# Kernel tuning notes

Measured on AMD Instinct MI355X. Metric: run time of the kernel, lower is better.

Reference implementation:

```python
import jax, jax.numpy as jnp
import numpy as np

BATCH, SEQ, DIM, NH = 2, 4096, 1024, 16
HD = DIM // NH
BLOCK = 64


def setup_inputs() -> dict:
    key = jax.random.key(0)
    ks = jax.random.split(key, 8)
    x = jax.random.normal(ks[0], (BATCH, SEQ, DIM), dtype=jnp.float32)
    # standard RoPE tables: (seq, head_dim)
    inv_freq = 1.0 / (10000.0 ** (jnp.arange(0, HD, 2, dtype=jnp.float32) / HD))
    t = jnp.arange(SEQ, dtype=jnp.float32)
    freqs = jnp.outer(t, inv_freq)                      # (SEQ, HD//2)
    emb = jnp.concatenate([freqs, freqs], axis=-1)      # (SEQ, HD)
    cos, sin = jnp.cos(emb), jnp.sin(emb)
    s = 0.02
    wq = jax.random.normal(ks[1], (DIM, DIM), jnp.float32) * s
    wk = jax.random.normal(ks[2], (DIM, DIM), jnp.float32) * s
    wv = jax.random.normal(ks[3], (DIM, DIM), jnp.float32) * s
    wo = jax.random.normal(ks[4], (DIM, DIM), jnp.float32) * s
    A_log = jax.random.normal(ks[5], (NH,), jnp.float32) * 0.1
    w_dt_w = jax.random.normal(ks[6], (DIM, NH), jnp.float32) * s
    w_dt_b = jnp.zeros((NH,), jnp.float32)
    return {"x": x, "cos": cos, "sin": sin, "wq": wq, "wk": wk, "wv": wv,
            "wo": wo, "A_log": A_log, "w_dt_w": w_dt_w, "w_dt_b": w_dt_b}


def segsum(a):
    """a: (..., T) -> (..., T, T) lower-triangular segment sums, -inf above diag."""
    T = a.shape[-1]
    cs = jnp.cumsum(a, axis=-1)
    seg = cs[..., :, None] - cs[..., None, :]
    mask = jnp.tril(jnp.ones((T, T), dtype=bool))
    return jnp.where(mask, seg, -jnp.inf)


def rotate_half(t):
    t1, t2 = jnp.split(t, 2, axis=-1)
    return jnp.concatenate([-t2, t1], axis=-1)


def ssd(X, A, B, C, block_len):
    """Mamba-2 SSD chunked scan.
    X: (b,l,h,p)  A: (b,l,h)  B,C: (b,l,h,n)
    """
    b, l, h, p = X.shape
    c = l // block_len
    Xc = X.reshape(b, c, block_len, h, p)
    Bc = B.reshape(b, c, block_len, h, -1)
    Cc = C.reshape(b, c, block_len, h, -1)
    Ac = jnp.transpose(A.reshape(b, c, block_len, h), (0, 3, 1, 2))  # (b,h,c,l)
    A_cumsum = jnp.cumsum(Ac, axis=-1)
    # intra-chunk (diagonal block) output
    L = jnp.exp(segsum(Ac))                                          # (b,h,c,l,l)
    Y_diag = jnp.einsum('bclhn,bcshn,bhcls,bcshp->bclhp', Cc, Bc, L, Xc)
    # per-chunk states
    decay_states = jnp.exp(A_cumsum[:, :, :, -1:] - A_cumsum)        # (b,h,c,l)
    states = jnp.einsum('bclhn,bhcl,bclhp->bchpn', Bc, decay_states, Xc)
    init = jnp.zeros_like(states[:, :1])
    states = jnp.concatenate([init, states], axis=1)                 # (b,c+1,h,p,n)
    # inter-chunk recurrence (done as a 1-SS matmul over chunk axis)
    A_last = jnp.pad(A_cumsum[:, :, :, -1], ((0, 0), (0, 0), (1, 0)))
    decay_chunk = jnp.exp(segsum(A_last))                            # (b,h,c+1,c+1)
    new_states = jnp.einsum('bhzc,bchpn->bzhpn', decay_chunk, states)
    states, final_state = new_states[:, :-1], new_states[:, -1]
    # state -> output contribution
    state_decay_out = jnp.exp(A_cumsum)
    Y_off = jnp.einsum('bclhn,bchpn,bhcl->bclhp', Cc, states, state_decay_out)
    Y = (Y_diag + Y_off).reshape(b, l, h, p)
    return Y, final_state


def reference(x, cos, sin, wq, wk, wv, wo, A_log, w_dt_w, w_dt_b):
    b, l, dim = x.shape
    h = A_log.shape[0]
    d = dim // h
    xq = (x @ wq).reshape(b, l, h, d)
    xk = (x @ wk).reshape(b, l, h, d)
    xv = (x @ wv).reshape(b, l, h, d)
    cb = cos[None, :, None, :]
    sb = sin[None, :, None, :]
    xq = xq * cb + rotate_half(xq) * sb
    xk = xk * cb + rotate_half(xk) * sb
    dt = jax.nn.softplus(x @ w_dt_w + w_dt_b)           # (b,l,h)
    A = -jnp.exp(A_log)[None, None, :] * dt             # (b,l,h)
    X = xv * dt[..., None]                              # (b,l,h,d)
    Y, state = ssd(X, A, xk, xq, BLOCK)
    # replicate torch's transpose(1,2).view(b, l, -1) exactly:
    y = jnp.transpose(Y, (0, 2, 1, 3)).reshape(b, l, h * d)
    return y @ wo, state
```

## Files before the change

### kernel.cpp

```cpp
#include <hip/hip_runtime.h>


typedef __bf16 bf16x8 __attribute__((ext_vector_type(8)));
typedef float f32x4 __attribute__((ext_vector_type(4)));
typedef unsigned int u32x4 __attribute__((ext_vector_type(4)));
typedef unsigned short u16x8 __attribute__((ext_vector_type(8)));
typedef unsigned short u16x4 __attribute__((ext_vector_type(4)));

__device__ __forceinline__ unsigned short f2bf(float f) {
  unsigned int u = __builtin_bit_cast(unsigned int, f);
  u += 0x7fffu + ((u >> 16) & 1u);
  return (unsigned short)(u >> 16);
}
__device__ __forceinline__ float bf2f(unsigned short s) {
  unsigned int u = ((unsigned int)s) << 16;
  return __builtin_bit_cast(float, u);
}

#define GLOAD16(gp, lp)                                                \
  __builtin_amdgcn_global_load_lds(                                    \
      (const __attribute__((address_space(1))) void*)(gp),             \
      (__attribute__((address_space(3))) void*)(lp), 16, 0, 0)

__global__ __launch_bounds__(256) void convert_bf16_kernel(
    const float* __restrict__ in, unsigned short* __restrict__ out, int n4) {
  int g = blockIdx.x * 256 + threadIdx.x;
  if (g < n4) {
    f32x4 v = *reinterpret_cast<const f32x4*>(in + (size_t)g * 4);
    u16x4 o;
    o.x = f2bf(v.x); o.y = f2bf(v.y); o.z = f2bf(v.z); o.w = f2bf(v.w);
    *reinterpret_cast<u16x4*>(out + (size_t)g * 4) = o;
  }
}

__global__ __launch_bounds__(256) void transpose_w_kernel(
    const float* __restrict__ w0, const float* __restrict__ w1,
    const float* __restrict__ w2, const float* __restrict__ w3,
    unsigned short* __restrict__ wt) {
  __shared__ float tile[32][33];
  const int z = blockIdx.z;
  const float* w = (z == 0) ? w0 : (z == 1) ? w1 : (z == 2) ? w2 : w3;
  unsigned short* o = wt + (size_t)z * 1024 * 1024;
  const int bx = blockIdx.x, by = blockIdx.y;
  const int tx = threadIdx.x, ty = threadIdx.y;
#pragma unroll
  for (int i = 0; i < 4; ++i)
    tile[ty + i * 8][tx] = w[(size_t)(by * 32 + ty + i * 8) * 1024 + bx * 32 + tx];
  __syncthreads();
#pragma unroll
  for (int i = 0; i < 4; ++i)
    o[(size_t)(bx * 32 + ty + i * 8) * 1024 + by * 32 + tx] = f2bf(tile[tx][ty + i * 8]);
}

__global__ __launch_bounds__(256) void wdt_t_kernel(
    const float* __restrict__ wdt, unsigned short* __restrict__ out) {
  const int g = blockIdx.x * 256 + threadIdx.x;
  const int n = g >> 10, k = g & 1023;
  out[g] = f2bf(wdt[k * 16 + n]);
}

__global__ __launch_bounds__(256) void dt_gemm_kernel(
    const unsigned short* __restrict__ A,
    const unsigned short* __restrict__ Bt,
    const float* __restrict__ bdt, float* __restrict__ dt) {
  __shared__ unsigned short As[2 * 64 * 32];
  const int tid = threadIdx.x, lane = tid & 63, w = tid >> 6;
  const int m0 = blockIdx.x * 64;
  const unsigned short* ga =
      A + (size_t)(m0 + w * 16 + (lane >> 2)) * 1024 + (lane & 3) * 8;
  unsigned short* la = As + w * 512;
  const int lr = lane & 15, lk = (lane >> 4) * 8;
  const unsigned short* gb = Bt + (size_t)lr * 1024 + lk;
  f32x4 acc = {};
  for (int kt = 0; kt < 1024; kt += 64) {
    GLOAD16(ga + kt, la);
    GLOAD16(ga + kt + 32, la + 2048);
    bf16x8 bF0 = *reinterpret_cast<const bf16x8*>(gb + kt);
    bf16x8 bF1 = *reinterpret_cast<const bf16x8*>(gb + kt + 32);
    __syncthreads();
    bf16x8 aF0 = *reinterpret_cast<const bf16x8*>(&As[(w * 16 + lr) * 32 + lk]);
    bf16x8 aF1 = *reinterpret_cast<const bf16x8*>(&As[2048 + (w * 16 + lr) * 32 + lk]);
    acc = __builtin_amdgcn_mfma_f32_16x16x32_bf16(aF0, bF0, acc, 0, 0, 0);
    acc = __builtin_amdgcn_mfma_f32_16x16x32_bf16(aF1, bF1, acc, 0, 0, 0);
    __syncthreads();
  }
  const int h = lr;
  const float bv = bdt[h];
#pragma unroll
  for (int r = 0; r < 4; ++r) {
    const int row = m0 + w * 16 + (lane >> 4) * 4 + r;
    const float a = acc[r] + bv;
    const float sp = (a > 0.f) ? (a + log1pf(expf(-a))) : log1pf(expf(a));
    dt[(size_t)row * 16 + h] = sp;
  }
}

template <int EPI>
__global__ __launch_bounds__(256) void gemm128_kernel(
    const unsigned short* __restrict__ A, const unsigned short* __restrict__ Bt,
    void* __restrict__ outp, const float* __restrict__ cosb,
    const float* __restrict__ sinb, const float* __restrict__ dtb) {
  __shared__ unsigned short As[128 * 32];
  __shared__ unsigned short Bs[128 * 32];
  const int tid = threadIdx.x, lane = tid & 63, w = tid >> 6;
  const int m0 = blockIdx.y * 128, n0 = blockIdx.x * 128;
  const int srow = w * 32 + (lane >> 2);
  const int scol = (lane & 3) * 8;
  const unsigned short* ga = A + (size_t)(m0 + srow) * 1024 + scol;
  const unsigned short* gb = Bt + (size_t)(n0 + srow) * 1024 + scol;
  unsigned short* la = As + (w * 32) * 32;
  unsigned short* lb = Bs + (w * 32) * 32;
  const int lr = lane & 15, lk = (lane >> 4) * 8;
  const int wr = w >> 1, wc = w & 1;
  f32x4 acc[4][4] = {};
  for (int kt = 0; kt < 1024; kt += 32) {
    GLOAD16(ga + kt, la);
    GLOAD16(ga + kt + (size_t)16 * 1024, la + 16 * 32);
    GLOAD16(gb + kt, lb);
    GLOAD16(gb + kt + (size_t)16 * 1024, lb + 16 * 32);
    __syncthreads();
    bf16x8 aF[4], bF[4];
#pragma unroll
    for (int i = 0; i < 4; ++i) {
      aF[i] = *reinterpret_cast<const bf16x8*>(&As[(wr * 64 + i * 16 + lr) * 32 + lk]);
      bF[i] = *reinterpret_cast<const bf16x8*>(&Bs[(wc * 64 + i * 16 + lr) * 32 + lk]);
    }
#pragma unroll
    for (int i = 0; i < 4; ++i)
#pragma unroll
      for (int j = 0; j < 4; ++j)
        acc[i][j] = __builtin_amdgcn_mfma_f32_16x16x32_bf16(aF[i], bF[j], acc[i][j], 0, 0, 0);
    __syncthreads();
  }
  const int r0 = m0 + wr * 64 + ((lane >> 4) << 2);
  const int c0 = n0 + wc * 64 + lr;
  if constexpr (EPI == 0) {
    float* O = (float*)outp;
#pragma unroll
    for (int i = 0; i < 4; ++i)
#pragma unroll
      for (int j = 0; j < 4; ++j)
#pragma unroll
        for (int r = 0; r < 4; ++r)
          O[(size_t)(r0 + i * 16 + r) * 1024 + c0 + j * 16] = acc[i][j][r];
  } else if constexpr (EPI == 1) {
    unsigned short* O = (unsigned short*)outp;
#pragma unroll
    for (int i = 0; i < 4; ++i)
#pragma unroll
      for (int jj = 0; jj < 2; ++jj) {
        const int d1 = jj * 16 + lr;
#pragma unroll
        for (int r = 0; r < 4; ++r) {
          const int row = r0 + i * 16 + r;
          const int l = row & 4095;
          const float cv = cosb[(size_t)l * 64 + d1];
          const float sv = sinb[(size_t)l * 64 + d1];
          const float v1 = acc[i][jj][r], v2 = acc[i][jj + 2][r];
          O[(size_t)row * 1024 + c0 + jj * 16] = f2bf(v1 * cv - v2 * sv);
          O[(size_t)row * 1024 + c0 + jj * 16 + 32] = f2bf(v2 * cv + v1 * sv);
        }
      }
  } else {
    unsigned short* O = (unsigned short*)outp;
    const int h = (n0 + wc * 64) >> 6;
#pragma unroll
    for (int i = 0; i < 4; ++i)
#pragma unroll
      for (int r = 0; r < 4; ++r) {
        const int row = r0 + i * 16 + r;
        const float dtv = dtb[(size_t)row * 16 + h];
#pragma unroll
        for (int j = 0; j < 4; ++j)
          O[(size_t)row * 1024 + c0 + j * 16] = f2bf(acc[i][j][r] * dtv);
      }
  }
}

__global__ __launch_bounds__(256) void ssd_states_kernel(
    const unsigned short* __restrict__ Kb, const unsigned short* __restrict__ Xb,
    const float* __restrict__ dtb, const float* __restrict__ A_log,
    unsigned short* __restrict__ chunk_states, float* __restrict__ chunk_dec) {
  __shared__ unsigned short T1[64 * 72], T2[64 * 72];
  __shared__ unsigned short BtL[64 * 72], XdL[64 * 72];
  __shared__ float csL[64], decL[64];
  const int c = blockIdx.x, h = blockIdx.y, b = blockIdx.z;
  const int tid = threadIdx.x, lane = tid & 63, w = tid >> 6;
  const size_t gbase = ((size_t)(b * 4096 + c * 64)) * 1024 + h * 64;
  {
    const int s = tid >> 2, e0 = (tid & 3) * 16;
    const unsigned short* gk = Kb + gbase + (size_t)s * 1024 + e0;
    const unsigned short* gx = Xb + gbase + (size_t)s * 1024 + e0;
    *(u32x4*)&T1[s * 72 + e0] = *(const u32x4*)gk;
    *(u32x4*)&T1[s * 72 + e0 + 8] = *(const u32x4*)(gk + 8);
    *(u32x4*)&T2[s * 72 + e0] = *(const u32x4*)gx;
    *(u32x4*)&T2[s * 72 + e0 + 8] = *(const u32x4*)(gx + 8);
  }
  if (w == 0) {
    float a = -expf(A_log[h]) * dtb[((size_t)(b * 4096 + c * 64 + lane)) * 16 + h];
    float v = a;
#pragma unroll
    for (int d = 1; d < 64; d <<= 1) {
      float o = __shfl_up(v, d, 64);
      if (lane >= d) v += o;
    }
    const float tot = __shfl(v, 63, 64);
    csL[lane] = v;
    decL[lane] = expf(tot - v);
    if (lane == 0) chunk_dec[((size_t)(b * 16 + h)) * 64 + c] = expf(tot);
  }
  __syncthreads();
#pragma unroll
  for (int q = 0; q < 2; ++q) {
    const int p = lane;
    const int s0 = (q * 4 + w) * 8;
    u16x8 vb, vx;
#pragma unroll
    for (int j = 0; j < 8; ++j) {
      vb[j] = T1[(s0 + j) * 72 + p];
      vx[j] = f2bf(bf2f(T2[(s0 + j) * 72 + p]) * decL[s0 + j]);
    }
    *(u16x8*)&BtL[p * 72 + s0] = vb;
    *(u16x8*)&XdL[p * 72 + s0] = vx;
  }
  __syncthreads();
  const int lr = lane & 15, lk = (lane >> 4) * 8;
  f32x4 acc[4] = {};
#pragma unroll
  for (int kt = 0; kt < 64; kt += 32) {
    bf16x8 aF = *reinterpret_cast<const bf16x8*>(&XdL[(w * 16 + lr) * 72 + kt + lk]);
#pragma unroll
    for (int j = 0; j < 4; ++j) {
      bf16x8 bF = *reinterpret_cast<const bf16x8*>(&BtL[(j * 16 + lr) * 72 + kt + lk]);
      acc[j] = __builtin_amdgcn_mfma_f32_16x16x32_bf16(aF, bF, acc[j], 0, 0, 0);
    }
  }
  const size_t stb = ((size_t)((b * 64 + c) * 16 + h)) * 4096;
#pragma unroll
  for (int j = 0; j < 4; ++j)
#pragma unroll
    for (int r = 0; r < 4; ++r)
      chunk_states[stb + (size_t)(w * 16 + (lane >> 4) * 4 + r) * 64 + j * 16 + lr] =
          f2bf(acc[j][r]);
}

__global__ __launch_bounds__(256) void scan_kernel(
    const unsigned short* __restrict__ chunk_states, const float* __restrict__ chunk_dec,
    unsigned short* __restrict__ inc_bf, float* __restrict__ state_out) {
  const int g = blockIdx.x * 256 + threadIdx.x;
  const int n = g & 63, p = (g >> 6) & 63, h = (g >> 12) & 15, b = g >> 16;
  const size_t pn = (size_t)p * 64 + n;
  float inc = 0.f;
  for (int c = 0; c < 64; ++c) {
    const size_t idx = ((size_t)((b * 64 + c) * 16 + h)) * 4096 + pn;
    inc_bf[idx] = f2bf(inc);
    inc = chunk_dec[(b * 16 + h) * 64 + c] * inc + bf2f(chunk_states[idx]);
  }
  state_out[((size_t)(b * 16 + h) * 64 + p) * 64 + n] = inc;
}

__global__ __launch_bounds__(256) void ssd_y_kernel(
    const unsigned short* __restrict__ Qb, const unsigned short* __restrict__ Kb,
    const unsigned short* __restrict__ Xb, const unsigned short* __restrict__ Sg,
    const float* __restrict__ dtb, const float* __restrict__ A_log,
    unsigned short* __restrict__ y_bf) {
  __shared__ unsigned short Cb[64 * 72], Bb[64 * 72], Sb[64 * 72];
  __shared__ unsigned short Xt[64 * 72], TG[64 * 72];
  __shared__ float csL[64], sdeL[64];
  const int c = blockIdx.x, h = blockIdx.y, b = blockIdx.z;
  const int tid = threadIdx.x, lane = tid & 63, w = tid >> 6;
  const size_t gbase = ((size_t)(b * 4096 + c * 64)) * 1024 + h * 64;
  const size_t sbase = ((size_t)((b * 64 + c) * 16 + h)) * 4096;
  {
    const int s = tid >> 2, e0 = (tid & 3) * 16;
    const unsigned short* gq = Qb + gbase + (size_t)s * 1024 + e0;
    const unsigned short* gk = Kb + gbase + (size_t)s * 1024 + e0;
    const unsigned short* gx = Xb + gbase + (size_t)s * 1024 + e0;
    const unsigned short* gs = Sg + sbase + (size_t)s * 64 + e0;
    *(u32x4*)&Cb[s * 72 + e0] = *(const u32x4*)gq;
    *(u32x4*)&Cb[s * 72 + e0 + 8] = *(const u32x4*)(gq + 8);
    *(u32x4*)&Bb[s * 72 + e0] = *(const u32x4*)gk;
    *(u32x4*)&Bb[s * 72 + e0 + 8] = *(const u32x4*)(gk + 8);
    *(u32x4*)&TG[s * 72 + e0] = *(const u32x4*)gx;
    *(u32x4*)&TG[s * 72 + e0 + 8] = *(const u32x4*)(gx + 8);
    *(u32x4*)&Sb[s * 72 + e0] = *(const u32x4*)gs;
    *(u32x4*)&Sb[s * 72 + e0 + 8] = *(const u32x4*)(gs + 8);
  }
  if (w == 0) {
    float a = -expf(A_log[h]) * dtb[((size_t)(b * 4096 + c * 64 + lane)) * 16 + h];
    float v = a;
#pragma unroll
    for (int d = 1; d < 64; d <<= 1) {
      float o = __shfl_up(v, d, 64);
      if (lane >= d) v += o;
    }
    csL[lane] = v;
    sdeL[lane] = expf(v);
  }
  __syncthreads();
  const int lr = lane & 15, lk = (lane >> 4) * 8;
  f32x4 g[4] = {};
#pragma unroll
  for (int kt = 0; kt < 64; kt += 32) {
    bf16x8 aF = *reinterpret_cast<const bf16x8*>(&Cb[(w * 16 + lr) * 72 + kt + lk]);
#pragma unroll
    for (int j = 0; j < 4; ++j) {
      bf16x8 bF = *reinterpret_cast<const bf16x8*>(&Bb[(j * 16 + lr) * 72 + kt + lk]);
      g[j] = __builtin_amdgcn_mfma_f32_16x16x32_bf16(aF, bF, g[j], 0, 0, 0);
    }
  }
#pragma unroll
  for (int q = 0; q < 2; ++q) {
    const int p = lane;
    const int s0 = (q * 4 + w) * 8;
    u16x8 vx;
#pragma unroll
    for (int j = 0; j < 8; ++j) vx[j] = TG[(s0 + j) * 72 + p];
    *(u16x8*)&Xt[p * 72 + s0] = vx;
  }
  __syncthreads();
#pragma unroll
  for (int j = 0; j < 4; ++j)
#pragma unroll
    for (int r = 0; r < 4; ++r) {
      const int l = w * 16 + (lane >> 4) * 4 + r;
      const int s = j * 16 + lr;
      const float gm = (l >= s) ? g[j][r] * expf(csL[l] - csL[s]) : 0.f;
      TG[l * 72 + s] = f2bf(gm);
    }
  {
    const int rl = tid >> 2, e0 = (tid & 3) * 16;
    const float sde = sdeL[rl];
#pragma unroll
    for (int half = 0; half < 2; ++half) {
      u16x8 v = *(u16x8*)&Cb[rl * 72 + e0 + half * 8];
#pragma unroll
      for (int j = 0; j < 8; ++j) v[j] = f2bf(bf2f(v[j]) * sde);
      *(u16x8*)&Cb[rl * 72 + e0 + half * 8] = v;
    }
  }
  __syncthreads();
  f32x4 acc[4] = {};
#pragma unroll
  for (int kt = 0; kt < 64; kt += 32) {
    bf16x8 aG = *reinterpret_cast<const bf16x8*>(&TG[(w * 16 + lr) * 72 + kt + lk]);
    bf16x8 aC = *reinterpret_cast<const bf16x8*>(&Cb[(w * 16 + lr) * 72 + kt + lk]);
#pragma unroll
    for (int j = 0; j < 4; ++j) {
      bf16x8 bX = *reinterpret_cast<const bf16x8*>(&Xt[(j * 16 + lr) * 72 + kt + lk]);
      bf16x8 bS = *reinterpret_cast<const bf16x8*>(&Sb[(j * 16 + lr) * 72 + kt + lk]);
      acc[j] = __builtin_amdgcn_mfma_f32_16x16x32_bf16(aG, bX, acc[j], 0, 0, 0);
      acc[j] = __builtin_amdgcn_mfma_f32_16x16x32_bf16(aC, bS, acc[j], 0, 0, 0);
    }
  }
  const size_t orow = (size_t)b * 4096 + h * 256 + c * 4 + w;
#pragma unroll
  for (int j = 0; j < 4; ++j)
#pragma unroll
    for (int r = 0; r < 4; ++r) {
      const int li = (lane >> 4) * 4 + r;
      y_bf[orow * 1024 + li * 64 + j * 16 + lr] = f2bf(acc[j][r]);
    }
}

extern "C" void kernel_launch(void* const* d_in, const int* in_sizes, int n_in,
                              void* d_out, int out_size, void* d_ws, size_t ws_size,
                              hipStream_t stream) {
  (void)in_sizes; (void)n_in; (void)out_size; (void)ws_size;
  const float* x = (const float*)d_in[0];
  const float* cosb = (const float*)d_in[1];
  const float* sinb = (const float*)d_in[2];
  const float* wq = (const float*)d_in[3];
  const float* wk = (const float*)d_in[4];
  const float* wv = (const float*)d_in[5];
  const float* wo = (const float*)d_in[6];
  const float* A_log = (const float*)d_in[7];
  const float* wdt = (const float*)d_in[8];
  const float* bdt = (const float*)d_in[9];

  float* out_y = (float*)d_out;
  float* out_state = out_y + 8388608;

  const size_t MBB = 1048576;
  char* ws = (char*)d_ws;
  unsigned short* x_bf = (unsigned short*)(ws);
  unsigned short* w_t = (unsigned short*)(ws + 16 * MBB);
  unsigned short* q_bf = (unsigned short*)(ws + 24 * MBB);
  unsigned short* k_bf = (unsigned short*)(ws + 40 * MBB);
  unsigned short* xv_bf = (unsigned short*)(ws + 56 * MBB);
  float* dtb = (float*)(ws + 72 * MBB);
  unsigned short* wdt_bf = (unsigned short*)(ws + 73 * MBB);
  unsigned short* chunk_states = (unsigned short*)(ws + 74 * MBB);
  float* chunk_dec = (float*)(ws + 90 * MBB);
  unsigned short* inc_bf = (unsigned short*)(ws + 91 * MBB);

  convert_bf16_kernel<<<8192, 256, 0, stream>>>(x, x_bf, 2097152);
  transpose_w_kernel<<<dim3(32, 32, 4), dim3(32, 8), 0, stream>>>(wq, wk, wv, wo, w_t);
  wdt_t_kernel<<<64, 256, 0, stream>>>(wdt, wdt_bf);
  dt_gemm_kernel<<<128, 256, 0, stream>>>(x_bf, wdt_bf, bdt, dtb);

  dim3 ggrid(8, 64);
  gemm128_kernel<1><<<ggrid, 256, 0, stream>>>(x_bf, w_t + 0 * MBB, q_bf, cosb, sinb, nullptr);
  gemm128_kernel<1><<<ggrid, 256, 0, stream>>>(x_bf, w_t + 1 * MBB, k_bf, cosb, sinb, nullptr);
  gemm128_kernel<2><<<ggrid, 256, 0, stream>>>(x_bf, w_t + 2 * MBB, xv_bf, nullptr, nullptr, dtb);

  ssd_states_kernel<<<dim3(64, 16, 2), 256, 0, stream>>>(k_bf, xv_bf, dtb, A_log,
                                                         chunk_states, chunk_dec);
  scan_kernel<<<512, 256, 0, stream>>>(chunk_states, chunk_dec, inc_bf, out_state);
  ssd_y_kernel<<<dim3(64, 16, 2), 256, 0, stream>>>(q_bf, k_bf, xv_bf, inc_bf, dtb, A_log,
                                                    x_bf );

  gemm128_kernel<0><<<ggrid, 256, 0, stream>>>(x_bf , w_t + 3 * MBB, out_y,
                                               nullptr, nullptr, nullptr);
}
```

Before: 191.3 us.

## Fuse QKV projections into one GEMM launch and merge small prep kernels

The three Q/K/V projection GEMMs become a single launch over a 24x64 grid that reads the stacked transposed weights. Each block picks its epilogue (RoPE into q or k, or dt scaling into v) from its column range. The w_dt transpose is folded into the x-to-bf16 conversion kernel as extra blocks. The scan kernel now caches the per-chunk decays in shared memory and prefetches the next chunk state. Together these cut launch count and tail effects, at the cost of a branchy epilogue and a dependence on the weights being stored contiguously.

```diff
diff --git a/kernel.cpp b/kernel.cpp
--- a/kernel.cpp
+++ b/kernel.cpp
@@ -23,13 +23,21 @@
       (__attribute__((address_space(3))) void*)(lp), 16, 0, 0)
 
 __global__ __launch_bounds__(256) void convert_bf16_kernel(
-    const float* __restrict__ in, unsigned short* __restrict__ out, int n4) {
-  int g = blockIdx.x * 256 + threadIdx.x;
-  if (g < n4) {
-    f32x4 v = *reinterpret_cast<const f32x4*>(in + (size_t)g * 4);
-    u16x4 o;
-    o.x = f2bf(v.x); o.y = f2bf(v.y); o.z = f2bf(v.z); o.w = f2bf(v.w);
-    *reinterpret_cast<u16x4*>(out + (size_t)g * 4) = o;
+    const float* __restrict__ in, unsigned short* __restrict__ out, int n4,
+    const float* __restrict__ wdt, unsigned short* __restrict__ wdt_bf) {
+  const int bx = blockIdx.x;
+  if (bx < 8192) {
+    int g = bx * 256 + threadIdx.x;
+    if (g < n4) {
+      f32x4 v = *reinterpret_cast<const f32x4*>(in + (size_t)g * 4);
+      u16x4 o;
+      o.x = f2bf(v.x); o.y = f2bf(v.y); o.z = f2bf(v.z); o.w = f2bf(v.w);
+      *reinterpret_cast<u16x4*>(out + (size_t)g * 4) = o;
+    }
+  } else {
+    const int g = (bx - 8192) * 256 + threadIdx.x;
+    const int n = g >> 10, k = g & 1023;
+    wdt_bf[g] = f2bf(wdt[k * 16 + n]);
   }
 }
 
@@ -50,13 +58,6 @@
 #pragma unroll
   for (int i = 0; i < 4; ++i)
     o[(size_t)(bx * 32 + ty + i * 8) * 1024 + by * 32 + tx] = f2bf(tile[tx][ty + i * 8]);
-}
-
-__global__ __launch_bounds__(256) void wdt_t_kernel(
-    const float* __restrict__ wdt, unsigned short* __restrict__ out) {
-  const int g = blockIdx.x * 256 + threadIdx.x;
-  const int n = g >> 10, k = g & 1023;
-  out[g] = f2bf(wdt[k * 16 + n]);
 }
 
 __global__ __launch_bounds__(256) void dt_gemm_kernel(
@@ -98,7 +99,8 @@
 template <int EPI>
 __global__ __launch_bounds__(256) void gemm128_kernel(
     const unsigned short* __restrict__ A, const unsigned short* __restrict__ Bt,
-    void* __restrict__ outp, const float* __restrict__ cosb,
+    void* __restrict__ out0, unsigned short* __restrict__ out1,
+    unsigned short* __restrict__ out2, const float* __restrict__ cosb,
     const float* __restrict__ sinb, const float* __restrict__ dtb) {
   __shared__ unsigned short As[128 * 32];
   __shared__ unsigned short Bs[128 * 32];
@@ -133,9 +135,9 @@
     __syncthreads();
   }
   const int r0 = m0 + wr * 64 + ((lane >> 4) << 2);
-  const int c0 = n0 + wc * 64 + lr;
   if constexpr (EPI == 0) {
-    float* O = (float*)outp;
+    float* O = (float*)out0;
+    const int c0 = n0 + wc * 64 + lr;
 #pragma unroll
     for (int i = 0; i < 4; ++i)
 #pragma unroll
@@ -143,37 +145,42 @@
 #pragma unroll
         for (int r = 0; r < 4; ++r)
           O[(size_t)(r0 + i * 16 + r) * 1024 + c0 + j * 16] = acc[i][j][r];
-  } else if constexpr (EPI == 1) {
-    unsigned short* O = (unsigned short*)outp;
-#pragma unroll
-    for (int i = 0; i < 4; ++i)
-#pragma unroll
-      for (int jj = 0; jj < 2; ++jj) {
-        const int d1 = jj * 16 + lr;
+  } else {
+    const int col = n0 + wc * 64;
+    if (col < 2048) {
+      unsigned short* O = (col < 1024) ? (unsigned short*)out0 : out1;
+      const int cbase = col & 1023;
+#pragma unroll
+      for (int i = 0; i < 4; ++i)
+#pragma unroll
+        for (int jj = 0; jj < 2; ++jj) {
+          const int d1 = jj * 16 + lr;
+#pragma unroll
+          for (int r = 0; r < 4; ++r) {
+            const int row = r0 + i * 16 + r;
+            const int l = row & 4095;
+            const float cv = cosb[(size_t)l * 64 + d1];
+            const float sv = sinb[(size_t)l * 64 + d1];
+            const float v1 = acc[i][jj][r], v2 = acc[i][jj + 2][r];
+            O[(size_t)row * 1024 + cbase + jj * 16 + lr] = f2bf(v1 * cv - v2 * sv);
+            O[(size_t)row * 1024 + cbase + jj * 16 + lr + 32] = f2bf(v2 * cv + v1 * sv);
+          }
+        }
+    } else {
+      unsigned short* O = out2;
+      const int cbase = col - 2048;
+      const int h = cbase >> 6;
+#pragma unroll
+      for (int i = 0; i < 4; ++i)
 #pragma unroll
         for (int r = 0; r < 4; ++r) {
           const int row = r0 + i * 16 + r;
-          const int l = row & 4095;
-          const float cv = cosb[(size_t)l * 64 + d1];
-          const float sv = sinb[(size_t)l * 64 + d1];
-          const float v1 = acc[i][jj][r], v2 = acc[i][jj + 2][r];
-          O[(size_t)row * 1024 + c0 + jj * 16] = f2bf(v1 * cv - v2 * sv);
-          O[(size_t)row * 1024 + c0 + jj * 16 + 32] = f2bf(v2 * cv + v1 * sv);
+          const float dtv = dtb[(size_t)row * 16 + h];
+#pragma unroll
+          for (int j = 0; j < 4; ++j)
+            O[(size_t)row * 1024 + cbase + j * 16 + lr] = f2bf(acc[i][j][r] * dtv);
         }
-      }
-  } else {
-    unsigned short* O = (unsigned short*)outp;
-    const int h = (n0 + wc * 64) >> 6;
-#pragma unroll
-    for (int i = 0; i < 4; ++i)
-#pragma unroll
-      for (int r = 0; r < 4; ++r) {
-        const int row = r0 + i * 16 + r;
-        const float dtv = dtb[(size_t)row * 16 + h];
-#pragma unroll
-        for (int j = 0; j < 4; ++j)
-          O[(size_t)row * 1024 + c0 + j * 16] = f2bf(acc[i][j][r] * dtv);
-      }
+    }
   }
 }
 
@@ -247,14 +254,24 @@
 __global__ __launch_bounds__(256) void scan_kernel(
     const unsigned short* __restrict__ chunk_states, const float* __restrict__ chunk_dec,
     unsigned short* __restrict__ inc_bf, float* __restrict__ state_out) {
+  __shared__ float decs[64];
   const int g = blockIdx.x * 256 + threadIdx.x;
   const int n = g & 63, p = (g >> 6) & 63, h = (g >> 12) & 15, b = g >> 16;
+  if (threadIdx.x < 64)
+    decs[threadIdx.x] = chunk_dec[(size_t)((blockIdx.x * 256) >> 12 & 15) * 64 +
+                                  (size_t)(blockIdx.x >> 8) * 1024 + threadIdx.x];
+  __syncthreads();
   const size_t pn = (size_t)p * 64 + n;
+  const size_t stride = (size_t)16 * 4096;
+  const size_t base0 = ((size_t)(b * 64) * 16 + h) * 4096 + pn;
   float inc = 0.f;
+  float cur = bf2f(chunk_states[base0]);
   for (int c = 0; c < 64; ++c) {
-    const size_t idx = ((size_t)((b * 64 + c) * 16 + h)) * 4096 + pn;
+    const size_t idx = base0 + (size_t)c * stride;
     inc_bf[idx] = f2bf(inc);
-    inc = chunk_dec[(b * 16 + h) * 64 + c] * inc + bf2f(chunk_states[idx]);
+    float nxt = (c < 63) ? bf2f(chunk_states[idx + stride]) : 0.f;
+    inc = decs[c] * inc + cur;
+    cur = nxt;
   }
   state_out[((size_t)(b * 16 + h) * 64 + p) * 64 + n] = inc;
 }
@@ -394,15 +411,12 @@
   float* chunk_dec = (float*)(ws + 90 * MBB);
   unsigned short* inc_bf = (unsigned short*)(ws + 91 * MBB);
 
-  convert_bf16_kernel<<<8192, 256, 0, stream>>>(x, x_bf, 2097152);
+  convert_bf16_kernel<<<8256, 256, 0, stream>>>(x, x_bf, 2097152, wdt, wdt_bf);
   transpose_w_kernel<<<dim3(32, 32, 4), dim3(32, 8), 0, stream>>>(wq, wk, wv, wo, w_t);
-  wdt_t_kernel<<<64, 256, 0, stream>>>(wdt, wdt_bf);
   dt_gemm_kernel<<<128, 256, 0, stream>>>(x_bf, wdt_bf, bdt, dtb);
 
-  dim3 ggrid(8, 64);
-  gemm128_kernel<1><<<ggrid, 256, 0, stream>>>(x_bf, w_t + 0 * MBB, q_bf, cosb, sinb, nullptr);
-  gemm128_kernel<1><<<ggrid, 256, 0, stream>>>(x_bf, w_t + 1 * MBB, k_bf, cosb, sinb, nullptr);
-  gemm128_kernel<2><<<ggrid, 256, 0, stream>>>(x_bf, w_t + 2 * MBB, xv_bf, nullptr, nullptr, dtb);
+  gemm128_kernel<3><<<dim3(24, 64), 256, 0, stream>>>(
+      x_bf, w_t, q_bf, k_bf, xv_bf, cosb, sinb, dtb);
 
   ssd_states_kernel<<<dim3(64, 16, 2), 256, 0, stream>>>(k_bf, xv_bf, dtb, A_log,
                                                          chunk_states, chunk_dec);
@@ -410,6 +424,6 @@
   ssd_y_kernel<<<dim3(64, 16, 2), 256, 0, stream>>>(q_bf, k_bf, xv_bf, inc_bf, dtb, A_log,
                                                     x_bf );
 
-  gemm128_kernel<0><<<ggrid, 256, 0, stream>>>(x_bf , w_t + 3 * MBB, out_y,
-                                               nullptr, nullptr, nullptr);
-}
+  gemm128_kernel<0><<<dim3(8, 64), 256, 0, stream>>>(
+      x_bf , w_t + 3 * MBB, out_y, nullptr, nullptr, nullptr, nullptr, nullptr);
+}
```

Result: faster. 180.1 us (-5.9%).
